# Performance work log

Measured on AMD Instinct MI355X. Metric: run time of the kernel, lower is better.

## Reference

```python
import jax, jax.numpy as jnp
import numpy as np

NBATCH, NSAMPLES, DIM, NHID, NLAYERS, DEG = 8, 2048, 4, 64, 3, 16
N = NBATCH * NSAMPLES
E = N * DEG
EPS = 1e-5


def setup_inputs() -> dict:
    key = jax.random.key(0)
    ks = jax.random.split(key, 16)
    x = jax.random.uniform(ks[0], (N, DIM), dtype=jnp.float32)
    # within-graph random edges (emulating radius_graph with contiguous batch)
    gid = jnp.repeat(jnp.arange(NBATCH, dtype=jnp.int64), NSAMPLES * DEG)
    src = jax.random.randint(ks[1], (E,), 0, NSAMPLES).astype(jnp.int64) + gid * NSAMPLES
    tgt = jax.random.randint(ks[2], (E,), 0, NSAMPLES).astype(jnp.int64) + gid * NSAMPLES
    edge_index = jnp.stack([src, tgt], axis=0)
    s = 0.05
    inp = {
        'x': x,
        'edge_index': edge_index,
        'enc_w': jax.random.normal(ks[3], (DIM, NHID), jnp.float32) * s,
        'enc_b': jnp.zeros((NHID,), jnp.float32),
        'm1_w': jax.random.normal(ks[4], (NLAYERS, 2 * NHID, NHID), jnp.float32) * s,
        'm1_b': jnp.zeros((NLAYERS, NHID), jnp.float32),
        'm2_w': jax.random.normal(ks[5], (NLAYERS, NHID, NHID), jnp.float32) * s,
        'm2_b': jnp.zeros((NLAYERS, NHID), jnp.float32),
        'u1_w': jax.random.normal(ks[6], (NLAYERS, NHID + NHID, NHID), jnp.float32) * s,
        'u1_b': jnp.zeros((NLAYERS, NHID), jnp.float32),
        'u2_w': jax.random.normal(ks[7], (NLAYERS, NHID, NHID), jnp.float32) * s,
        'u2_b': jnp.zeros((NLAYERS, NHID), jnp.float32),
        'dec_w': jax.random.normal(ks[8], (NHID, DIM), jnp.float32) * s,
        'dec_b': jnp.zeros((DIM,), jnp.float32),
    }
    return inp


def _l2star_sq(X):
    # Warnock formula for squared L2-star discrepancy, per graph.
    # X: [B, n, d] in [0,1]
    n = X.shape[1]
    d = X.shape[2]
    t1 = (1.0 / 3.0) ** d
    prod1 = jnp.prod(1.0 - X * X, axis=-1)          # [B, n]
    t2 = prod1.sum(axis=-1) * (2.0 / (n * (2.0 ** d)))
    # pairwise prod_k (1 - max(x_ik, x_jk)); loop over small d to avoid [B,n,n,d]
    acc = jnp.ones((X.shape[0], n, n), X.dtype)
    for k in range(d):
        acc = acc * (1.0 - jnp.maximum(X[:, :, None, k], X[:, None, :, k]))
    t3 = acc.sum(axis=(-1, -2)) / (n * n)
    return t1 - t2 + t3  # [B]


def _forward(x, edge_index, enc_w, enc_b, m1_w, m1_b, m2_w, m2_b,
             u1_w, u1_b, u2_w, u2_b, dec_w, dec_b):
    src, tgt = edge_index[0], edge_index[1]
    h = x @ enc_w + enc_b  # [N, NHID]
    for l in range(NLAYERS):
        x_j = h[src]  # source features
        x_i = h[tgt]  # target features
        m = jax.nn.relu(jnp.concatenate([x_i, x_j], axis=-1) @ m1_w[l] + m1_b[l])
        m = jax.nn.relu(m @ m2_w[l] + m2_b[l])
        agg = jax.ops.segment_sum(m, tgt, num_segments=N)  # default aggr='add'
        h = jax.nn.relu(jnp.concatenate([h, agg], axis=-1) @ u1_w[l] + u1_b[l])
        h = jax.nn.relu(h @ u2_w[l] + u2_b[l])
        # InstanceNorm per graph (batch is contiguous blocks of NSAMPLES)
        hb = h.reshape(NBATCH, NSAMPLES, NHID)
        mean = hb.mean(axis=1, keepdims=True)
        var = hb.var(axis=1, keepdims=True)
        h = ((hb - mean) * jax.lax.rsqrt(var + EPS)).reshape(N, NHID)
    X = jax.nn.sigmoid(h @ dec_w + dec_b).reshape(NBATCH, NSAMPLES, DIM)
    loss = jnp.mean(_l2star_sq(X))
    return loss, X


def reference(x, edge_index, enc_w, enc_b, m1_w, m1_b, m2_w, m2_b,
              u1_w, u1_b, u2_w, u2_b, dec_w, dec_b):
    return _forward(x, edge_index, enc_w, enc_b, m1_w, m1_b, m2_w, m2_b,
                    u1_w, u1_b, u2_w, u2_b, dec_w, dec_b)
```

## Files before the change

### kernel.cpp

```cpp
#include <hip/hip_runtime.h>
#include <hip/hip_fp16.h>
#include <math.h>

#define NB 8
#define NS 2048
#define NN (NB*NS)
#define NE (NN*16)
#define EPSF 1e-5f

typedef float  f32x4 __attribute__((ext_vector_type(4)));
typedef _Float16 f16x8 __attribute__((ext_vector_type(8)));
union F8 { f16x8 v; unsigned u[4]; };

__device__ __forceinline__ unsigned pk2h(float a, float b) {
    __half2 hh = __floats2half2_rn(a, b);
    unsigned u; __builtin_memcpy(&u, &hh, 4); return u;
}

__global__ __launch_bounds__(256) void k_init(int* __restrict__ deg,
                                              float* __restrict__ acc)
{
    int i = blockIdx.x*256 + threadIdx.x;
    if (i < NN) deg[i] = 0;
    if (i < 4) acc[i] = 0.f;
}

__global__ __launch_bounds__(256) void k_pre0M(
    const float* __restrict__ x,
    const float* __restrict__ encW, const float* __restrict__ encB,
    float* __restrict__ h,
    const float* __restrict__ W1, const float* __restrict__ B1,
    float* __restrict__ A, float* __restrict__ Bm,
    float* __restrict__ gz,
    const int* __restrict__ srcv, const int* __restrict__ tgtv,
    int* __restrict__ deg, int* __restrict__ ssrc)
{
    alignas(16) __shared__ _Float16 sWp[8192];
    __shared__ float sEw[256], sEb[64];
    {
        int gid = blockIdx.x*256 + threadIdx.x;
        #pragma unroll
        for (int it = 0; it < 4; it++) {
            int e = gid + it*65536;
            int t = tgtv[e];
            int pos = atomicAdd(&deg[t], 1) & 63;
            ssrc[t*64 + pos] = srcv[e];
        }
    }
    for (int idx = threadIdx.x; idx < 8192; idx += 256) {
        int k = idx >> 7, n = idx & 127;
        float val = (n < 64) ? W1[k*64 + n] : W1[(64+k)*64 + (n-64)];
        int ks = k >> 5, qd = (k >> 3) & 3, j = k & 7, nt = n >> 4, cl = n & 15;
        sWp[(((ks*8+nt)*4+qd)*16+cl)*8 + j] = (_Float16)val;
    }
    sEw[threadIdx.x] = encW[threadIdx.x];
    if (threadIdx.x < 64) sEb[threadIdx.x] = encB[threadIdx.x];
    if (blockIdx.x == 0)
        for (int i = threadIdx.x; i < 2*NB*64; i += 256) gz[i] = 0.f;
    __syncthreads();
    const int lane = threadIdx.x & 63;
    const int wv = threadIdx.x >> 6;
    const int col = lane & 15, quad = lane >> 4;
    const int n0w = blockIdx.x*64 + wv*16;
    const int n = n0w + col;
    float4 x4 = *(const float4*)&x[(size_t)n*4];
    float xv[16];
    #pragma unroll
    for (int hh = 0; hh < 2; hh++)
        #pragma unroll
        for (int j = 0; j < 8; j++) {
            int f = hh*32 + quad*8 + j;
            float v = sEb[f];
            v = fmaf(x4.x, sEw[f],     v);
            v = fmaf(x4.y, sEw[64+f],  v);
            v = fmaf(x4.z, sEw[128+f], v);
            v = fmaf(x4.w, sEw[192+f], v);
            xv[hh*8+j] = v;
        }
    float* hp = &h[(size_t)n*64 + quad*8];
    *(float4*)&hp[0]  = *(float4*)&xv[0];
    *(float4*)&hp[4]  = *(float4*)&xv[4];
    *(float4*)&hp[32] = *(float4*)&xv[8];
    *(float4*)&hp[36] = *(float4*)&xv[12];
    F8 af0, af1;
    af0.u[0] = pk2h(xv[0],  xv[1]);  af0.u[1] = pk2h(xv[2],  xv[3]);
    af0.u[2] = pk2h(xv[4],  xv[5]);  af0.u[3] = pk2h(xv[6],  xv[7]);
    af1.u[0] = pk2h(xv[8],  xv[9]);  af1.u[1] = pk2h(xv[10], xv[11]);
    af1.u[2] = pk2h(xv[12], xv[13]); af1.u[3] = pk2h(xv[14], xv[15]);
    float b1v[4];
    #pragma unroll
    for (int nt = 0; nt < 4; nt++) b1v[nt] = B1[nt*16+col];
    #pragma unroll
    for (int nt = 0; nt < 8; nt++) {
        f32x4 acc = {0.f,0.f,0.f,0.f};
        F8 bf; bf.v = *(const f16x8*)&sWp[(((0*8+nt)*4+quad)*16+col)*8];
        acc = __builtin_amdgcn_mfma_f32_16x16x32_f16(af0.v, bf.v, acc, 0, 0, 0);
        bf.v = *(const f16x8*)&sWp[(((1*8+nt)*4+quad)*16+col)*8];
        acc = __builtin_amdgcn_mfma_f32_16x16x32_f16(af1.v, bf.v, acc, 0, 0, 0);
        if (nt < 4) {
            float bb = b1v[nt];
            A[(size_t)(n0w + quad*4 + 0)*64 + nt*16 + col] = acc.x + bb;
            A[(size_t)(n0w + quad*4 + 1)*64 + nt*16 + col] = acc.y + bb;
            A[(size_t)(n0w + quad*4 + 2)*64 + nt*16 + col] = acc.z + bb;
            A[(size_t)(n0w + quad*4 + 3)*64 + nt*16 + col] = acc.w + bb;
        } else {
            Bm[(size_t)(n0w + quad*4 + 0)*64 + (nt-4)*16 + col] = acc.x;
            Bm[(size_t)(n0w + quad*4 + 1)*64 + (nt-4)*16 + col] = acc.y;
            Bm[(size_t)(n0w + quad*4 + 2)*64 + (nt-4)*16 + col] = acc.z;
            Bm[(size_t)(n0w + quad*4 + 3)*64 + (nt-4)*16 + col] = acc.w;
        }
    }
}

__global__ __launch_bounds__(256, 4) void k_eu(
    const float* __restrict__ A, const float* __restrict__ Bm,
    const int* __restrict__ deg, const int* __restrict__ ssrc,
    const float* __restrict__ W2e, const float* __restrict__ B2e,
    float* __restrict__ h,
    const float* __restrict__ W1u, const float* __restrict__ B1u,
    const float* __restrict__ W2u, const float* __restrict__ B2u,
    float* __restrict__ gout)
{
    alignas(16) __shared__ _Float16 sW1u[8192];
    alignas(16) __shared__ _Float16 sW2u[4096];
    alignas(16) __shared__ _Float16 sM2[4096];
    alignas(16) __shared__ float sAgg[16*68];
    for (int idx = threadIdx.x; idx < 8192; idx += 256) {
        int k = idx >> 6, n = idx & 63;
        int ks = k >> 5, qd = (k >> 3) & 3, j = k & 7, nt = n >> 4, cl = n & 15;
        sW1u[(((ks*4+nt)*4+qd)*16+cl)*8 + j] = (_Float16)W1u[idx];
    }
    for (int idx = threadIdx.x; idx < 4096; idx += 256) {
        int k = idx >> 6, n = idx & 63;
        int ks = k >> 5, qd = (k >> 3) & 3, j = k & 7, nt = n >> 4, cl = n & 15;
        sW2u[(((ks*4+nt)*4+qd)*16+cl)*8 + j] = (_Float16)W2u[idx];
        sM2 [(((ks*4+nt)*4+qd)*16+cl)*8 + j] = (_Float16)W2e[idx];
    }
    __syncthreads();
    const int lane = threadIdx.x & 63;
    const int wv = threadIdx.x >> 6;
    const int col = lane & 15, quad = lane >> 4;
    F8 bfe[4][2];
    #pragma unroll
    for (int nt = 0; nt < 4; nt++)
        #pragma unroll
        for (int ks = 0; ks < 2; ks++)
            bfe[nt][ks].v = *(const f16x8*)&sM2[(((ks*4+nt)*4+quad)*16+col)*8];
    float b2e[4];
    #pragma unroll
    for (int nt = 0; nt < 4; nt++) b2e[nt] = B2e[nt*16 + col];

    const int t_base = blockIdx.x * 16;
    int cnts[4], sv[4];
    #pragma unroll
    for (int m = 0; m < 4; m++) {
        int t = t_base + wv*4 + m;
        cnts[m] = deg[t];
        sv[m] = ssrc[t*64 + lane];
    }
    #pragma unroll
    for (int m = 0; m < 4; m++) {
        int t = t_base + wv*4 + m;
        int cnt = cnts[m] > 64 ? 64 : cnts[m];
        const float* ar = &A[(size_t)t*64 + quad*8];
        float4 a0 = *(const float4*)&ar[0];
        float4 a1 = *(const float4*)&ar[4];
        float4 a2 = *(const float4*)&ar[32];
        float4 a3 = *(const float4*)&ar[36];
        float cs[4] = {0.f, 0.f, 0.f, 0.f};
        for (int s0 = 0; s0 < cnt; s0 += 16) {
            int v = cnt - s0;
            int cc = col < v-1 ? col : v-1;
            int sr = __shfl(sv[m], s0 + cc, 64);
            const float* br = &Bm[(size_t)sr*64 + quad*8];
            float4 b0 = *(const float4*)&br[0];
            float4 b1 = *(const float4*)&br[4];
            float4 b2_ = *(const float4*)&br[32];
            float4 b3 = *(const float4*)&br[36];
            F8 af0, af1;
            af0.u[0] = pk2h(fmaxf(a0.x+b0.x,0.f), fmaxf(a0.y+b0.y,0.f));
            af0.u[1] = pk2h(fmaxf(a0.z+b0.z,0.f), fmaxf(a0.w+b0.w,0.f));
            af0.u[2] = pk2h(fmaxf(a1.x+b1.x,0.f), fmaxf(a1.y+b1.y,0.f));
            af0.u[3] = pk2h(fmaxf(a1.z+b1.z,0.f), fmaxf(a1.w+b1.w,0.f));
            af1.u[0] = pk2h(fmaxf(a2.x+b2_.x,0.f), fmaxf(a2.y+b2_.y,0.f));
            af1.u[1] = pk2h(fmaxf(a2.z+b2_.z,0.f), fmaxf(a2.w+b2_.w,0.f));
            af1.u[2] = pk2h(fmaxf(a3.x+b3.x,0.f), fmaxf(a3.y+b3.y,0.f));
            af1.u[3] = pk2h(fmaxf(a3.z+b3.z,0.f), fmaxf(a3.w+b3.w,0.f));
            #pragma unroll
            for (int nt = 0; nt < 4; nt++) {
                f32x4 acc = __builtin_amdgcn_mfma_f32_16x16x32_f16(
                                af0.v, bfe[nt][0].v, (f32x4){0.f,0.f,0.f,0.f}, 0, 0, 0);
                acc = __builtin_amdgcn_mfma_f32_16x16x32_f16(
                                af1.v, bfe[nt][1].v, acc, 0, 0, 0);
                float r0 = (quad*4+0 < v) ? fmaxf(acc.x + b2e[nt], 0.f) : 0.f;
                float r1 = (quad*4+1 < v) ? fmaxf(acc.y + b2e[nt], 0.f) : 0.f;
                float r2 = (quad*4+2 < v) ? fmaxf(acc.z + b2e[nt], 0.f) : 0.f;
                float r3 = (quad*4+3 < v) ? fmaxf(acc.w + b2e[nt], 0.f) : 0.f;
                cs[nt] += (r0 + r1) + (r2 + r3);
            }
        }
        #pragma unroll
        for (int nt = 0; nt < 4; nt++) {
            float vv = cs[nt];
            vv += __shfl_down(vv, 32, 64);
            vv += __shfl_down(vv, 16, 64);
            cs[nt] = vv;
        }
        if (lane < 16) {
            sAgg[(wv*4+m)*68 +  0 + lane] = cs[0];
            sAgg[(wv*4+m)*68 + 16 + lane] = cs[1];
            sAgg[(wv*4+m)*68 + 32 + lane] = cs[2];
            sAgg[(wv*4+m)*68 + 48 + lane] = cs[3];
        }
    }
    __syncthreads();
    if (wv == 0) {
        const int n0w = t_base;
        const float* hp = &h[(size_t)(n0w+col)*64 + quad*8];
        float4 h0 = *(const float4*)&hp[0];
        float4 h1 = *(const float4*)&hp[4];
        float4 h2 = *(const float4*)&hp[32];
        float4 h3 = *(const float4*)&hp[36];
        const float* ap = &sAgg[col*68 + quad*8];
        float4 g0 = *(const float4*)&ap[0];
        float4 g1 = *(const float4*)&ap[4];
        float4 g2 = *(const float4*)&ap[32];
        float4 g3 = *(const float4*)&ap[36];
        F8 af[4];
        af[0].u[0] = pk2h(h0.x, h0.y); af[0].u[1] = pk2h(h0.z, h0.w);
        af[0].u[2] = pk2h(h1.x, h1.y); af[0].u[3] = pk2h(h1.z, h1.w);
        af[1].u[0] = pk2h(h2.x, h2.y); af[1].u[1] = pk2h(h2.z, h2.w);
        af[1].u[2] = pk2h(h3.x, h3.y); af[1].u[3] = pk2h(h3.z, h3.w);
        af[2].u[0] = pk2h(g0.x, g0.y); af[2].u[1] = pk2h(g0.z, g0.w);
        af[2].u[2] = pk2h(g1.x, g1.y); af[2].u[3] = pk2h(g1.z, g1.w);
        af[3].u[0] = pk2h(g2.x, g2.y); af[3].u[1] = pk2h(g2.z, g2.w);
        af[3].u[2] = pk2h(g3.x, g3.y); af[3].u[3] = pk2h(g3.z, g3.w);
        float b1v[4], b2v[4];
        #pragma unroll
        for (int nt = 0; nt < 4; nt++) { b1v[nt] = B1u[nt*16+col]; b2v[nt] = B2u[nt*16+col]; }
        #pragma unroll
        for (int nt = 0; nt < 4; nt++) {
            f32x4 acc = {0.f,0.f,0.f,0.f};
            #pragma unroll
            for (int ks = 0; ks < 4; ks++) {
                F8 bf; bf.v = *(const f16x8*)&sW1u[(((ks*4+nt)*4+quad)*16+col)*8];
                acc = __builtin_amdgcn_mfma_f32_16x16x32_f16(af[ks].v, bf.v, acc, 0, 0, 0);
            }
            sAgg[(quad*4+0)*68 + nt*16+col] = fmaxf(acc.x + b1v[nt], 0.f);
            sAgg[(quad*4+1)*68 + nt*16+col] = fmaxf(acc.y + b1v[nt], 0.f);
            sAgg[(quad*4+2)*68 + nt*16+col] = fmaxf(acc.z + b1v[nt], 0.f);
            sAgg[(quad*4+3)*68 + nt*16+col] = fmaxf(acc.w + b1v[nt], 0.f);
        }
        const float* hr = &sAgg[col*68 + quad*8];
        float4 q0 = *(const float4*)&hr[0];
        float4 q1 = *(const float4*)&hr[4];
        float4 q2 = *(const float4*)&hr[32];
        float4 q3 = *(const float4*)&hr[36];
        F8 e0, e1;
        e0.u[0] = pk2h(q0.x, q0.y); e0.u[1] = pk2h(q0.z, q0.w);
        e0.u[2] = pk2h(q1.x, q1.y); e0.u[3] = pk2h(q1.z, q1.w);
        e1.u[0] = pk2h(q2.x, q2.y); e1.u[1] = pk2h(q2.z, q2.w);
        e1.u[2] = pk2h(q3.x, q3.y); e1.u[3] = pk2h(q3.z, q3.w);
        float ss[4], sq[4];
        #pragma unroll
        for (int nt = 0; nt < 4; nt++) {
            f32x4 acc = {0.f,0.f,0.f,0.f};
            F8 bf; bf.v = *(const f16x8*)&sW2u[(((0*4+nt)*4+quad)*16+col)*8];
            acc = __builtin_amdgcn_mfma_f32_16x16x32_f16(e0.v, bf.v, acc, 0, 0, 0);
            bf.v = *(const f16x8*)&sW2u[(((1*4+nt)*4+quad)*16+col)*8];
            acc = __builtin_amdgcn_mfma_f32_16x16x32_f16(e1.v, bf.v, acc, 0, 0, 0);
            float o0 = fmaxf(acc.x + b2v[nt], 0.f);
            float o1 = fmaxf(acc.y + b2v[nt], 0.f);
            float o2 = fmaxf(acc.z + b2v[nt], 0.f);
            float o3 = fmaxf(acc.w + b2v[nt], 0.f);
            h[(size_t)(n0w + quad*4 + 0)*64 + nt*16 + col] = o0;
            h[(size_t)(n0w + quad*4 + 1)*64 + nt*16 + col] = o1;
            h[(size_t)(n0w + quad*4 + 2)*64 + nt*16 + col] = o2;
            h[(size_t)(n0w + quad*4 + 3)*64 + nt*16 + col] = o3;
            ss[nt] = (o0 + o1) + (o2 + o3);
            sq[nt] = (o0*o0 + o1*o1) + (o2*o2 + o3*o3);
        }
        #pragma unroll
        for (int nt = 0; nt < 4; nt++) {
            float v = ss[nt];
            v += __shfl_down(v, 32, 64); v += __shfl_down(v, 16, 64);
            ss[nt] = v;
            float w2 = sq[nt];
            w2 += __shfl_down(w2, 32, 64); w2 += __shfl_down(w2, 16, 64);
            sq[nt] = w2;
        }
        if (lane < 16) {
            int b = (int)(blockIdx.x >> 7);
            #pragma unroll
            for (int nt = 0; nt < 4; nt++) {
                atomicAdd(&gout[b*64 + nt*16 + lane], ss[nt]);
                atomicAdd(&gout[NB*64 + b*64 + nt*16 + lane], sq[nt]);
            }
        }
    }
}

__global__ __launch_bounds__(256) void k_preM(
    float* __restrict__ h,
    const float* __restrict__ W1, const float* __restrict__ B1,
    float* __restrict__ A, float* __restrict__ Bm,
    const float* __restrict__ gin, float* __restrict__ gz)
{
    alignas(16) __shared__ _Float16 sWp[8192];
    __shared__ float sMean[64], sRstd[64];
    for (int idx = threadIdx.x; idx < 8192; idx += 256) {
        int k = idx >> 7, n = idx & 127;
        float val = (n < 64) ? W1[k*64 + n] : W1[(64+k)*64 + (n-64)];
        int ks = k >> 5, qd = (k >> 3) & 3, j = k & 7, nt = n >> 4, cl = n & 15;
        sWp[(((ks*8+nt)*4+qd)*16+cl)*8 + j] = (_Float16)val;
    }
    if (threadIdx.x < 64) {
        int b = (int)(blockIdx.x >> 5);
        float s  = gin[b*64 + threadIdx.x];
        float qq = gin[NB*64 + b*64 + threadIdx.x];
        float mean = s * (1.f/NS);
        float var  = qq * (1.f/NS) - mean*mean;
        sMean[threadIdx.x] = mean;
        sRstd[threadIdx.x] = rsqrtf(var + EPSF);
    }
    if (blockIdx.x == 0)
        for (int i = threadIdx.x; i < 2*NB*64; i += 256) gz[i] = 0.f;
    __syncthreads();
    const int lane = threadIdx.x & 63;
    const int wv = threadIdx.x >> 6;
    const int col = lane & 15, quad = lane >> 4;
    const int n0w = blockIdx.x*64 + wv*16;
    float* hp = &h[(size_t)(n0w+col)*64 + quad*8];
    float xv[16];
    *(float4*)&xv[0]  = *(const float4*)&hp[0];
    *(float4*)&xv[4]  = *(const float4*)&hp[4];
    *(float4*)&xv[8]  = *(const float4*)&hp[32];
    *(float4*)&xv[12] = *(const float4*)&hp[36];
    #pragma unroll
    for (int t2 = 0; t2 < 8; t2++) {
        int f = quad*8 + t2;
        xv[t2] = (xv[t2] - sMean[f]) * sRstd[f];
    }
    #pragma unroll
    for (int t2 = 0; t2 < 8; t2++) {
        int f = 32 + quad*8 + t2;
        xv[8+t2] = (xv[8+t2] - sMean[f]) * sRstd[f];
    }
    *(float4*)&hp[0]  = *(float4*)&xv[0];
    *(float4*)&hp[4]  = *(float4*)&xv[4];
    *(float4*)&hp[32] = *(float4*)&xv[8];
    *(float4*)&hp[36] = *(float4*)&xv[12];
    F8 af0, af1;
    af0.u[0] = pk2h(xv[0],  xv[1]);  af0.u[1] = pk2h(xv[2],  xv[3]);
    af0.u[2] = pk2h(xv[4],  xv[5]);  af0.u[3] = pk2h(xv[6],  xv[7]);
    af1.u[0] = pk2h(xv[8],  xv[9]);  af1.u[1] = pk2h(xv[10], xv[11]);
    af1.u[2] = pk2h(xv[12], xv[13]); af1.u[3] = pk2h(xv[14], xv[15]);
    float b1v[4];
    #pragma unroll
    for (int nt = 0; nt < 4; nt++) b1v[nt] = B1[nt*16+col];
    #pragma unroll
    for (int nt = 0; nt < 8; nt++) {
        f32x4 acc = {0.f,0.f,0.f,0.f};
        F8 bf; bf.v = *(const f16x8*)&sWp[(((0*8+nt)*4+quad)*16+col)*8];
        acc = __builtin_amdgcn_mfma_f32_16x16x32_f16(af0.v, bf.v, acc, 0, 0, 0);
        bf.v = *(const f16x8*)&sWp[(((1*8+nt)*4+quad)*16+col)*8];
        acc = __builtin_amdgcn_mfma_f32_16x16x32_f16(af1.v, bf.v, acc, 0, 0, 0);
        if (nt < 4) {
            float bb = b1v[nt];
            A[(size_t)(n0w + quad*4 + 0)*64 + nt*16 + col] = acc.x + bb;
            A[(size_t)(n0w + quad*4 + 1)*64 + nt*16 + col] = acc.y + bb;
            A[(size_t)(n0w + quad*4 + 2)*64 + nt*16 + col] = acc.z + bb;
            A[(size_t)(n0w + quad*4 + 3)*64 + nt*16 + col] = acc.w + bb;
        } else {
            Bm[(size_t)(n0w + quad*4 + 0)*64 + (nt-4)*16 + col] = acc.x;
            Bm[(size_t)(n0w + quad*4 + 1)*64 + (nt-4)*16 + col] = acc.y;
            Bm[(size_t)(n0w + quad*4 + 2)*64 + (nt-4)*16 + col] = acc.z;
            Bm[(size_t)(n0w + quad*4 + 3)*64 + (nt-4)*16 + col] = acc.w;
        }
    }
}

__global__ __launch_bounds__(256) void k_dec(
    const float* __restrict__ h, const float* __restrict__ Wd, const float* __restrict__ bd,
    const float* __restrict__ g, float* __restrict__ xbuf, float* __restrict__ out1,
    float* __restrict__ accum)
{
    int n = blockIdx.x*256 + threadIdx.x;
    int b = n >> 11;
    __shared__ float sM[64], sR[64];
    __shared__ float sWd[256];
    if (threadIdx.x < 64) {
        float s  = g[b*64 + threadIdx.x];
        float qq = g[NB*64 + b*64 + threadIdx.x];
        float mean = s * (1.f/NS);
        float var  = qq * (1.f/NS) - mean*mean;
        sM[threadIdx.x] = mean; sR[threadIdx.x] = rsqrtf(var + EPSF);
    }
    for (int i = threadIdx.x; i < 256; i += 256) sWd[i] = Wd[i];
    __syncthreads();
    float a0 = bd[0], a1 = bd[1], a2 = bd[2], a3 = bd[3];
    const float* hr = h + (size_t)n*64;
    #pragma unroll 8
    for (int k = 0; k < 64; k++) {
        float v = (hr[k] - sM[k]) * sR[k];
        a0 = fmaf(v, sWd[k*4+0], a0);
        a1 = fmaf(v, sWd[k*4+1], a1);
        a2 = fmaf(v, sWd[k*4+2], a2);
        a3 = fmaf(v, sWd[k*4+3], a3);
    }
    float4 o;
    o.x = 1.f/(1.f + expf(-a0));
    o.y = 1.f/(1.f + expf(-a1));
    o.z = 1.f/(1.f + expf(-a2));
    o.w = 1.f/(1.f + expf(-a3));
    *(float4*)&xbuf[(size_t)n*4] = o;
    out1[n*4+0] = o.x; out1[n*4+1] = o.y; out1[n*4+2] = o.z; out1[n*4+3] = o.w;
    float p = (1.f-o.x*o.x)*(1.f-o.y*o.y)*(1.f-o.z*o.z)*(1.f-o.w*o.w);
    for (int offs = 32; offs; offs >>= 1) p += __shfl_down(p, offs, 64);
    __shared__ float ws[4];
    if ((threadIdx.x & 63) == 0) ws[threadIdx.x >> 6] = p;
    __syncthreads();
    if (threadIdx.x == 0) atomicAdd(&accum[0], ws[0]+ws[1]+ws[2]+ws[3]);
}

__global__ __launch_bounds__(256) void k_t3(const float* __restrict__ X,
                                            float* __restrict__ accum,
                                            float* __restrict__ out)
{
    int b = blockIdx.x >> 5, c = blockIdx.x & 31;
    __shared__ float sX[NS*4];
    const float* Xb = X + (size_t)b*NS*4;
    for (int idx = threadIdx.x; idx < NS*4; idx += 256) sX[idx] = Xb[idx];
    __syncthreads();
    const float4* sX4 = (const float4*)sX;
    int il = threadIdx.x & 63, wv = threadIdx.x >> 6;
    float4 xi = sX4[c*64 + il];
    float acc = 0.f;
    #pragma unroll 4
    for (int s = 0; s < 512; s++) {
        float4 xj = sX4[wv*512 + s];
        acc += (1.f - fmaxf(xi.x, xj.x)) * (1.f - fmaxf(xi.y, xj.y))
             * (1.f - fmaxf(xi.z, xj.z)) * (1.f - fmaxf(xi.w, xj.w));
    }
    for (int offs = 32; offs; offs >>= 1) acc += __shfl_down(acc, offs, 64);
    __shared__ float ws[4];
    if (il == 0) ws[wv] = acc;
    __syncthreads();
    if (threadIdx.x == 0) {
        atomicAdd(&accum[1], ws[0]+ws[1]+ws[2]+ws[3]);
        __threadfence();
        unsigned t = atomicAdd((unsigned int*)&accum[2], 1u);
        if (t == (unsigned)(NB*32 - 1)) {
            float A2 = __hip_atomic_load(&accum[0], __ATOMIC_ACQUIRE, __HIP_MEMORY_SCOPE_AGENT);
            float A3 = __hip_atomic_load(&accum[1], __ATOMIC_ACQUIRE, __HIP_MEMORY_SCOPE_AGENT);
            float t1 = 1.f/81.f;
            float t2 = (2.f/(NS*16.f)) * (A2 / NB);
            float t3 = (A3 / ((float)NS*(float)NS)) / NB;
            out[0] = t1 - t2 + t3;
        }
    }
}

extern "C" void kernel_launch(void* const* d_in, const int* in_sizes, int n_in,
                              void* d_out, int out_size, void* d_ws, size_t ws_size,
                              hipStream_t stream)
{
    const float* x     = (const float*)d_in[0];
    const int*   ei    = (const int*)d_in[1];
    const float* enc_w = (const float*)d_in[2];
    const float* enc_b = (const float*)d_in[3];
    const float* m1w   = (const float*)d_in[4];
    const float* m1b   = (const float*)d_in[5];
    const float* m2w   = (const float*)d_in[6];
    const float* m2b   = (const float*)d_in[7];
    const float* u1w   = (const float*)d_in[8];
    const float* u1b   = (const float*)d_in[9];
    const float* u2w   = (const float*)d_in[10];
    const float* u2b   = (const float*)d_in[11];
    const float* dw    = (const float*)d_in[12];
    const float* db    = (const float*)d_in[13];
    float* out = (float*)d_out;

    float* h    = (float*)d_ws;
    float* Apre = h    + NN*64;
    float* Bpre = Apre + NN*64;
    float* g0   = Bpre + NN*64;
    float* g1   = g0   + 2*NB*64;
    float* acc  = g1   + 2*NB*64;
    int*   deg  = (int*)(acc + 4);
    int*   ssrc = deg + NN;
    float* xbuf = Apre;

    const int* srcv = ei;
    const int* tgtv = ei + NE;
    float* gbuf[2] = {g0, g1};

    k_init<<<NN/256, 256, 0, stream>>>(deg, acc);
    k_pre0M<<<NN/64, 256, 0, stream>>>(x, enc_w, enc_b, h, m1w, m1b,
                                       Apre, Bpre, g0, srcv, tgtv, deg, ssrc);

    for (int l = 0; l < 3; l++) {
        if (l)
            k_preM<<<NN/64, 256, 0, stream>>>(h, m1w + l*128*64, m1b + l*64,
                                              Apre, Bpre,
                                              gbuf[(l+1)&1], gbuf[l&1]);
        k_eu<<<NN/16, 256, 0, stream>>>(Apre, Bpre, deg, ssrc,
                                        m2w + l*64*64, m2b + l*64,
                                        h,
                                        u1w + l*128*64, u1b + l*64,
                                        u2w + l*64*64,  u2b + l*64,
                                        gbuf[l&1]);
    }

    k_dec<<<NN/256, 256, 0, stream>>>(h, dw, db, g0, xbuf, out + 1, acc);
    k_t3<<<NB*32, 256, 0, stream>>>(xbuf, acc, out);
}
```

Before: 229.6 us.

## Split node-update MLP across all waves; retune decoder and t3 grid sizes

The node-update MLP tail in k_eu, previously run by wave 0 alone, is now split so that each of the four waves computes one 16-column output tile, with added block barriers between stages. k_dec is relaunched with 64-thread blocks, which drops the shared-memory cross-wave reduction. k_t3 now has each thread handle two i-points, halving the grid and reusing each loaded x_j twice. Together these aim to cut serialized single-wave work and shared-memory traffic, in exchange for extra syncs and fewer k_t3 blocks to fill the GPU.

```diff
diff --git a/kernel.cpp b/kernel.cpp
--- a/kernel.cpp
+++ b/kernel.cpp
@@ -214,43 +214,43 @@
         }
     }
     __syncthreads();
-    if (wv == 0) {
-        const int n0w = t_base;
-        const float* hp = &h[(size_t)(n0w+col)*64 + quad*8];
-        float4 h0 = *(const float4*)&hp[0];
-        float4 h1 = *(const float4*)&hp[4];
-        float4 h2 = *(const float4*)&hp[32];
-        float4 h3 = *(const float4*)&hp[36];
-        const float* ap = &sAgg[col*68 + quad*8];
-        float4 g0 = *(const float4*)&ap[0];
-        float4 g1 = *(const float4*)&ap[4];
-        float4 g2 = *(const float4*)&ap[32];
-        float4 g3 = *(const float4*)&ap[36];
-        F8 af[4];
-        af[0].u[0] = pk2h(h0.x, h0.y); af[0].u[1] = pk2h(h0.z, h0.w);
-        af[0].u[2] = pk2h(h1.x, h1.y); af[0].u[3] = pk2h(h1.z, h1.w);
-        af[1].u[0] = pk2h(h2.x, h2.y); af[1].u[1] = pk2h(h2.z, h2.w);
-        af[1].u[2] = pk2h(h3.x, h3.y); af[1].u[3] = pk2h(h3.z, h3.w);
-        af[2].u[0] = pk2h(g0.x, g0.y); af[2].u[1] = pk2h(g0.z, g0.w);
-        af[2].u[2] = pk2h(g1.x, g1.y); af[2].u[3] = pk2h(g1.z, g1.w);
-        af[3].u[0] = pk2h(g2.x, g2.y); af[3].u[1] = pk2h(g2.z, g2.w);
-        af[3].u[2] = pk2h(g3.x, g3.y); af[3].u[3] = pk2h(g3.z, g3.w);
-        float b1v[4], b2v[4];
+    const int n0w = t_base;
+    const float* hp = &h[(size_t)(n0w+col)*64 + quad*8];
+    float4 h0 = *(const float4*)&hp[0];
+    float4 h1 = *(const float4*)&hp[4];
+    float4 h2 = *(const float4*)&hp[32];
+    float4 h3 = *(const float4*)&hp[36];
+    const float* ap = &sAgg[col*68 + quad*8];
+    float4 g0 = *(const float4*)&ap[0];
+    float4 g1 = *(const float4*)&ap[4];
+    float4 g2 = *(const float4*)&ap[32];
+    float4 g3 = *(const float4*)&ap[36];
+    F8 af[4];
+    af[0].u[0] = pk2h(h0.x, h0.y); af[0].u[1] = pk2h(h0.z, h0.w);
+    af[0].u[2] = pk2h(h1.x, h1.y); af[0].u[3] = pk2h(h1.z, h1.w);
+    af[1].u[0] = pk2h(h2.x, h2.y); af[1].u[1] = pk2h(h2.z, h2.w);
+    af[1].u[2] = pk2h(h3.x, h3.y); af[1].u[3] = pk2h(h3.z, h3.w);
+    af[2].u[0] = pk2h(g0.x, g0.y); af[2].u[1] = pk2h(g0.z, g0.w);
+    af[2].u[2] = pk2h(g1.x, g1.y); af[2].u[3] = pk2h(g1.z, g1.w);
+    af[3].u[0] = pk2h(g2.x, g2.y); af[3].u[1] = pk2h(g2.z, g2.w);
+    af[3].u[2] = pk2h(g3.x, g3.y); af[3].u[3] = pk2h(g3.z, g3.w);
+    const float b1v = B1u[wv*16+col];
+    const float b2v = B2u[wv*16+col];
+    __syncthreads();
+    {
+        f32x4 acc = {0.f,0.f,0.f,0.f};
         #pragma unroll
-        for (int nt = 0; nt < 4; nt++) { b1v[nt] = B1u[nt*16+col]; b2v[nt] = B2u[nt*16+col]; }
-        #pragma unroll
-        for (int nt = 0; nt < 4; nt++) {
-            f32x4 acc = {0.f,0.f,0.f,0.f};
-            #pragma unroll
-            for (int ks = 0; ks < 4; ks++) {
-                F8 bf; bf.v = *(const f16x8*)&sW1u[(((ks*4+nt)*4+quad)*16+col)*8];
-                acc = __builtin_amdgcn_mfma_f32_16x16x32_f16(af[ks].v, bf.v, acc, 0, 0, 0);
-            }
-            sAgg[(quad*4+0)*68 + nt*16+col] = fmaxf(acc.x + b1v[nt], 0.f);
-            sAgg[(quad*4+1)*68 + nt*16+col] = fmaxf(acc.y + b1v[nt], 0.f);
-            sAgg[(quad*4+2)*68 + nt*16+col] = fmaxf(acc.z + b1v[nt], 0.f);
-            sAgg[(quad*4+3)*68 + nt*16+col] = fmaxf(acc.w + b1v[nt], 0.f);
-        }
+        for (int ks = 0; ks < 4; ks++) {
+            F8 bf; bf.v = *(const f16x8*)&sW1u[(((ks*4+wv)*4+quad)*16+col)*8];
+            acc = __builtin_amdgcn_mfma_f32_16x16x32_f16(af[ks].v, bf.v, acc, 0, 0, 0);
+        }
+        sAgg[(quad*4+0)*68 + wv*16+col] = fmaxf(acc.x + b1v, 0.f);
+        sAgg[(quad*4+1)*68 + wv*16+col] = fmaxf(acc.y + b1v, 0.f);
+        sAgg[(quad*4+2)*68 + wv*16+col] = fmaxf(acc.z + b1v, 0.f);
+        sAgg[(quad*4+3)*68 + wv*16+col] = fmaxf(acc.w + b1v, 0.f);
+    }
+    __syncthreads();
+    {
         const float* hr = &sAgg[col*68 + quad*8];
         float4 q0 = *(const float4*)&hr[0];
         float4 q1 = *(const float4*)&hr[4];
@@ -261,41 +261,27 @@
         e0.u[2] = pk2h(q1.x, q1.y); e0.u[3] = pk2h(q1.z, q1.w);
         e1.u[0] = pk2h(q2.x, q2.y); e1.u[1] = pk2h(q2.z, q2.w);
         e1.u[2] = pk2h(q3.x, q3.y); e1.u[3] = pk2h(q3.z, q3.w);
-        float ss[4], sq[4];
-        #pragma unroll
-        for (int nt = 0; nt < 4; nt++) {
-            f32x4 acc = {0.f,0.f,0.f,0.f};
-            F8 bf; bf.v = *(const f16x8*)&sW2u[(((0*4+nt)*4+quad)*16+col)*8];
-            acc = __builtin_amdgcn_mfma_f32_16x16x32_f16(e0.v, bf.v, acc, 0, 0, 0);
-            bf.v = *(const f16x8*)&sW2u[(((1*4+nt)*4+quad)*16+col)*8];
-            acc = __builtin_amdgcn_mfma_f32_16x16x32_f16(e1.v, bf.v, acc, 0, 0, 0);
-            float o0 = fmaxf(acc.x + b2v[nt], 0.f);
-            float o1 = fmaxf(acc.y + b2v[nt], 0.f);
-            float o2 = fmaxf(acc.z + b2v[nt], 0.f);
-            float o3 = fmaxf(acc.w + b2v[nt], 0.f);
-            h[(size_t)(n0w + quad*4 + 0)*64 + nt*16 + col] = o0;
-            h[(size_t)(n0w + quad*4 + 1)*64 + nt*16 + col] = o1;
-            h[(size_t)(n0w + quad*4 + 2)*64 + nt*16 + col] = o2;
-            h[(size_t)(n0w + quad*4 + 3)*64 + nt*16 + col] = o3;
-            ss[nt] = (o0 + o1) + (o2 + o3);
-            sq[nt] = (o0*o0 + o1*o1) + (o2*o2 + o3*o3);
-        }
-        #pragma unroll
-        for (int nt = 0; nt < 4; nt++) {
-            float v = ss[nt];
-            v += __shfl_down(v, 32, 64); v += __shfl_down(v, 16, 64);
-            ss[nt] = v;
-            float w2 = sq[nt];
-            w2 += __shfl_down(w2, 32, 64); w2 += __shfl_down(w2, 16, 64);
-            sq[nt] = w2;
-        }
+        f32x4 acc = {0.f,0.f,0.f,0.f};
+        F8 bf; bf.v = *(const f16x8*)&sW2u[(((0*4+wv)*4+quad)*16+col)*8];
+        acc = __builtin_amdgcn_mfma_f32_16x16x32_f16(e0.v, bf.v, acc, 0, 0, 0);
+        bf.v = *(const f16x8*)&sW2u[(((1*4+wv)*4+quad)*16+col)*8];
+        acc = __builtin_amdgcn_mfma_f32_16x16x32_f16(e1.v, bf.v, acc, 0, 0, 0);
+        float o0 = fmaxf(acc.x + b2v, 0.f);
+        float o1 = fmaxf(acc.y + b2v, 0.f);
+        float o2 = fmaxf(acc.z + b2v, 0.f);
+        float o3 = fmaxf(acc.w + b2v, 0.f);
+        h[(size_t)(n0w + quad*4 + 0)*64 + wv*16 + col] = o0;
+        h[(size_t)(n0w + quad*4 + 1)*64 + wv*16 + col] = o1;
+        h[(size_t)(n0w + quad*4 + 2)*64 + wv*16 + col] = o2;
+        h[(size_t)(n0w + quad*4 + 3)*64 + wv*16 + col] = o3;
+        float ss = (o0 + o1) + (o2 + o3);
+        float sq = (o0*o0 + o1*o1) + (o2*o2 + o3*o3);
+        ss += __shfl_down(ss, 32, 64); ss += __shfl_down(ss, 16, 64);
+        sq += __shfl_down(sq, 32, 64); sq += __shfl_down(sq, 16, 64);
         if (lane < 16) {
             int b = (int)(blockIdx.x >> 7);
-            #pragma unroll
-            for (int nt = 0; nt < 4; nt++) {
-                atomicAdd(&gout[b*64 + nt*16 + lane], ss[nt]);
-                atomicAdd(&gout[NB*64 + b*64 + nt*16 + lane], sq[nt]);
-            }
+            atomicAdd(&gout[b*64 + wv*16 + lane], ss);
+            atomicAdd(&gout[NB*64 + b*64 + wv*16 + lane], sq);
         }
     }
 }
@@ -380,23 +366,23 @@
     }
 }
 
-__global__ __launch_bounds__(256) void k_dec(
+__global__ __launch_bounds__(64) void k_dec(
     const float* __restrict__ h, const float* __restrict__ Wd, const float* __restrict__ bd,
     const float* __restrict__ g, float* __restrict__ xbuf, float* __restrict__ out1,
     float* __restrict__ accum)
 {
-    int n = blockIdx.x*256 + threadIdx.x;
+    int n = blockIdx.x*64 + threadIdx.x;
     int b = n >> 11;
     __shared__ float sM[64], sR[64];
     __shared__ float sWd[256];
-    if (threadIdx.x < 64) {
+    {
         float s  = g[b*64 + threadIdx.x];
         float qq = g[NB*64 + b*64 + threadIdx.x];
         float mean = s * (1.f/NS);
         float var  = qq * (1.f/NS) - mean*mean;
         sM[threadIdx.x] = mean; sR[threadIdx.x] = rsqrtf(var + EPSF);
     }
-    for (int i = threadIdx.x; i < 256; i += 256) sWd[i] = Wd[i];
+    for (int i = threadIdx.x; i < 256; i += 64) sWd[i] = Wd[i];
     __syncthreads();
     float a0 = bd[0], a1 = bd[1], a2 = bd[2], a3 = bd[3];
     const float* hr = h + (size_t)n*64;
@@ -417,31 +403,32 @@
     out1[n*4+0] = o.x; out1[n*4+1] = o.y; out1[n*4+2] = o.z; out1[n*4+3] = o.w;
     float p = (1.f-o.x*o.x)*(1.f-o.y*o.y)*(1.f-o.z*o.z)*(1.f-o.w*o.w);
     for (int offs = 32; offs; offs >>= 1) p += __shfl_down(p, offs, 64);
-    __shared__ float ws[4];
-    if ((threadIdx.x & 63) == 0) ws[threadIdx.x >> 6] = p;
-    __syncthreads();
-    if (threadIdx.x == 0) atomicAdd(&accum[0], ws[0]+ws[1]+ws[2]+ws[3]);
+    if (threadIdx.x == 0) atomicAdd(&accum[0], p);
 }
 
 __global__ __launch_bounds__(256) void k_t3(const float* __restrict__ X,
                                             float* __restrict__ accum,
                                             float* __restrict__ out)
 {
-    int b = blockIdx.x >> 5, c = blockIdx.x & 31;
+    int b = blockIdx.x >> 4, c = blockIdx.x & 15;
     __shared__ float sX[NS*4];
     const float* Xb = X + (size_t)b*NS*4;
     for (int idx = threadIdx.x; idx < NS*4; idx += 256) sX[idx] = Xb[idx];
     __syncthreads();
     const float4* sX4 = (const float4*)sX;
     int il = threadIdx.x & 63, wv = threadIdx.x >> 6;
-    float4 xi = sX4[c*64 + il];
-    float acc = 0.f;
+    float4 xiA = sX4[(c*2+0)*64 + il];
+    float4 xiB = sX4[(c*2+1)*64 + il];
+    float accA = 0.f, accB = 0.f;
     #pragma unroll 4
     for (int s = 0; s < 512; s++) {
         float4 xj = sX4[wv*512 + s];
-        acc += (1.f - fmaxf(xi.x, xj.x)) * (1.f - fmaxf(xi.y, xj.y))
-             * (1.f - fmaxf(xi.z, xj.z)) * (1.f - fmaxf(xi.w, xj.w));
-    }
+        accA += (1.f - fmaxf(xiA.x, xj.x)) * (1.f - fmaxf(xiA.y, xj.y))
+              * (1.f - fmaxf(xiA.z, xj.z)) * (1.f - fmaxf(xiA.w, xj.w));
+        accB += (1.f - fmaxf(xiB.x, xj.x)) * (1.f - fmaxf(xiB.y, xj.y))
+              * (1.f - fmaxf(xiB.z, xj.z)) * (1.f - fmaxf(xiB.w, xj.w));
+    }
+    float acc = accA + accB;
     for (int offs = 32; offs; offs >>= 1) acc += __shfl_down(acc, offs, 64);
     __shared__ float ws[4];
     if (il == 0) ws[wv] = acc;
@@ -450,7 +437,7 @@
         atomicAdd(&accum[1], ws[0]+ws[1]+ws[2]+ws[3]);
         __threadfence();
         unsigned t = atomicAdd((unsigned int*)&accum[2], 1u);
-        if (t == (unsigned)(NB*32 - 1)) {
+        if (t == (unsigned)(NB*16 - 1)) {
             float A2 = __hip_atomic_load(&accum[0], __ATOMIC_ACQUIRE, __HIP_MEMORY_SCOPE_AGENT);
             float A3 = __hip_atomic_load(&accum[1], __ATOMIC_ACQUIRE, __HIP_MEMORY_SCOPE_AGENT);
             float t1 = 1.f/81.f;
@@ -512,6 +499,6 @@
                                         gbuf[l&1]);
     }
 
-    k_dec<<<NN/256, 256, 0, stream>>>(h, dw, db, g0, xbuf, out + 1, acc);
-    k_t3<<<NB*32, 256, 0, stream>>>(xbuf, acc, out);
-}
+    k_dec<<<NN/64, 64, 0, stream>>>(h, dw, db, g0, xbuf, out + 1, acc);
+    k_t3<<<NB*16, 256, 0, stream>>>(xbuf, acc, out);
+}
```

New measurement: 237.4 us. 1.03x slower.
